# Performance work log

Hardware: AMD Instinct MI355X
Metric: run time of the kernel (lower is better)

The kernel has to match this reference:

```python
import jax, jax.numpy as jnp
import numpy as np

D = 256  # channel dim and CBP output dim


def setup_inputs() -> dict:
    key = jax.random.key(0)
    ks = jax.random.split(key, 14)
    B, C, H, W = 32, 256, 56, 56
    attr_num = 400
    inp = {}
    inp["entity_feature"] = jax.random.normal(ks[0], (B, C, H, W), jnp.float32)
    inp["attr_one_hot"] = jax.random.uniform(ks[1], (B, attr_num), jnp.float32)
    # textual_emb: Linear(attr_num, 256)
    inp["W_emb"] = jax.random.normal(ks[2], (D, attr_num), jnp.float32) * 0.02
    inp["b_emb"] = jnp.zeros((D,), jnp.float32)
    # conv: Conv2d(256,256,1)
    inp["conv_w"] = jax.random.normal(ks[3], (D, D), jnp.float32) * 0.02
    inp["conv_b"] = jnp.zeros((D,), jnp.float32)
    # mcb_conv1_attr: Conv2d(256,32,1)
    inp["conv1_w"] = jax.random.normal(ks[4], (32, D), jnp.float32) * 0.05
    inp["conv1_b"] = jnp.zeros((32,), jnp.float32)
    # mcb_conv2_attr: Conv2d(32,1,1)
    inp["conv2_w"] = jax.random.normal(ks[5], (1, 32), jnp.float32) * 0.1
    inp["conv2_b"] = jnp.zeros((1,), jnp.float32)
    # CompactBilinearPooling count-sketch tables (fixed random at init)
    inp["h1"] = jax.random.randint(ks[6], (D,), 0, D, jnp.int32)
    inp["h2"] = jax.random.randint(ks[7], (D,), 0, D, jnp.int32)
    inp["s1"] = (jax.random.randint(ks[8], (D,), 0, 2, jnp.int32) * 2 - 1).astype(jnp.float32)
    inp["s2"] = (jax.random.randint(ks[9], (D,), 0, 2, jnp.int32) * 2 - 1).astype(jnp.float32)
    return inp


def _sketch_matrix(h, s):
    # sparse count-sketch projection as dense [C_in, D] matrix: P[i, h[i]] = s[i]
    return jnp.zeros((D, D), jnp.float32).at[jnp.arange(D), h].add(s)


def reference(entity_feature, attr_one_hot, W_emb, b_emb, conv_w, conv_b,
              conv1_w, conv1_b, conv2_w, conv2_b, h1, h2, s1, s2):
    feature = jax.nn.relu(entity_feature)                      # [B,256,H,W]
    # textual embedding + spatially-constant 1x1 conv (identical math to
    # expanding then convolving, since the expanded tensor is constant over HxW)
    t = attr_one_hot @ W_emb.T + b_emb                         # [B,256]
    a = t @ conv_w.T + conv_b                                  # [B,256]

    # Compact Bilinear Pooling (count sketch -> FFT -> elementwise mul -> iFFT)
    P1 = _sketch_matrix(h1, s1)
    P2 = _sketch_matrix(h2, s2)
    sk1 = a @ P1                                               # [B,256], spatially constant
    sk2 = jnp.einsum('bchw,cd->bdhw', feature, P2)             # [B,256,H,W]
    fft1 = jnp.fft.rfft(sk1, n=D, axis=1)[:, :, None, None]    # [B,129,1,1]
    fft2 = jnp.fft.rfft(sk2, n=D, axis=1)                      # [B,129,H,W]
    mcb = jnp.fft.irfft(fft1 * fft2, n=D, axis=1)              # [B,256,H,W]

    # gating chain: conv1x1 -> relu -> conv1x1 -> sigmoid
    x = jax.nn.relu(jnp.einsum('bchw,oc->bohw', mcb, conv1_w) + conv1_b[None, :, None, None])
    attr_map = jax.nn.sigmoid(jnp.einsum('bchw,oc->bohw', x, conv2_w) + conv2_b[None, :, None, None])  # [B,1,H,W]
    attr_feature = attr_map * entity_feature                   # [B,256,H,W]
    return attr_map, attr_feature
```

## Files before the change

### kernel.cpp

```cpp
#include <hip/hip_runtime.h>

#define Dq    256
#define ATTR  400
#define HW    3136
#define NB    32
#define PXT   112
#define NPX4  28
#define PITCH 116
#define NTILE 28

typedef __attribute__((ext_vector_type(8))) short bf16x8;
typedef __attribute__((ext_vector_type(4))) float f32x4;

__device__ __forceinline__ unsigned short f2bf(float f) {
  unsigned int x = __float_as_uint(f);
  return (unsigned short)((x + 0x7FFFu + ((x >> 16) & 1u)) >> 16);
}
__device__ __forceinline__ float bf2f(unsigned int u) {
  return __uint_as_float(u << 16);
}

__global__ __launch_bounds__(256) void k_sk1(
    const float* __restrict__ oh, const float* __restrict__ W_emb,
    const float* __restrict__ b_emb, const float* __restrict__ conv_w,
    const float* __restrict__ conv_b, const int* __restrict__ h1,
    const float* __restrict__ s1, float* __restrict__ sk1_out) {
  __shared__ float ohs[ATTR];
  __shared__ float ts[Dq];
  __shared__ float sk[Dq];
  const int b = blockIdx.x, tid = threadIdx.x;
  for (int j = tid; j < ATTR; j += 256) ohs[j] = oh[b * ATTR + j];
  sk[tid] = 0.f;
  __syncthreads();
  float acc = b_emb[tid];
  const float* wr = W_emb + tid * ATTR;
  for (int j = 0; j < ATTR; ++j) acc = fmaf(ohs[j], wr[j], acc);
  ts[tid] = acc;
  __syncthreads();
  float a = conv_b[tid];
  const float* cr = conv_w + tid * Dq;
  for (int k = 0; k < Dq; ++k) a = fmaf(ts[k], cr[k], a);
  atomicAdd(&sk[h1[tid]], a * s1[tid]);
  __syncthreads();
  sk1_out[b * Dq + tid] = sk[tid];
}

__global__ __launch_bounds__(256) void k_G(
    const float* __restrict__ sk1, const float* __restrict__ conv1_w,
    const int* __restrict__ h2, const float* __restrict__ s2,
    unsigned short* __restrict__ Abuf) {
  __shared__ float sks[Dq];
  __shared__ float w1[Dq];
  __shared__ float Tl[Dq];
  const int b = blockIdx.x >> 5, o = blockIdx.x & 31, c = threadIdx.x;
  sks[c] = sk1[b * Dq + c];
  w1[c]  = conv1_w[o * Dq + c];
  __syncthreads();
  float t = 0.f;
  for (int d = 0; d < Dq; ++d) t = fmaf(w1[d], sks[(d - c) & 255], t);
  Tl[c] = t;
  __syncthreads();
  const float g = s2[c] * Tl[h2[c]];
  const int frag = (o >> 4) * 8 + (c >> 5);
  const int lane = (o & 15) | (((c >> 3) & 3) << 4);
  Abuf[(((size_t)b * 16 + frag) * 64 + lane) * 8 + (c & 7)] = f2bf(g);
}

__global__ __launch_bounds__(448, 4) void k_tile(
    const float* __restrict__ ent,
    const unsigned short* __restrict__ Abuf,
    const float* __restrict__ c1b, const float* __restrict__ c2w,
    const float* __restrict__ c2b,
    float* __restrict__ out)
{
  __shared__ unsigned short tile[Dq * PITCH];
  __shared__ float s_lds[PXT];
  const int b = blockIdx.y;
  const int px_base = blockIdx.x * PXT;
  const int t = threadIdx.x;
  const int c0 = t / NPX4;
  const int fi = t % NPX4;

  const float* eb = ent + (size_t)b * Dq * HW + px_base;

#pragma unroll
  for (int k = 0; k < 16; ++k) {
    const int c = 16 * k + c0;
    f32x4 v = *reinterpret_cast<const f32x4*>(eb + (size_t)c * HW + 4 * fi);
    unsigned int d0 = (unsigned int)f2bf(v[0]) | ((unsigned int)f2bf(v[1]) << 16);
    unsigned int d1 = (unsigned int)f2bf(v[2]) | ((unsigned int)f2bf(v[3]) << 16);
    uint2 dv; dv.x = d0; dv.y = d1;
    *reinterpret_cast<uint2*>(&tile[c * PITCH + 4 * fi]) = dv;
  }
  __syncthreads();

  const int w = t >> 6, l = t & 63;
  const int n = l & 15, kg = l >> 4;
  const unsigned short* Ab = Abuf + ((size_t)b * 16 * 64 + l) * 8;

  f32x4 acc0 = {0.f, 0.f, 0.f, 0.f}, acc1 = {0.f, 0.f, 0.f, 0.f};
#pragma unroll
  for (int ks = 0; ks < 8; ++ks) {
    unsigned short uv[8];
#pragma unroll
    for (int j = 0; j < 8; ++j)
      uv[j] = tile[(ks * 32 + kg * 8 + j) * PITCH + w * 16 + n];
    bf16x8 bv;
#pragma unroll
    for (int j = 0; j < 8; ++j)
      bv[j] = (short)((uv[j] & 0x8000u) ? 0u : (unsigned int)uv[j]);
    bf16x8 a0 = *reinterpret_cast<const bf16x8*>(Ab + (size_t)(0 * 8 + ks) * 64 * 8);
    bf16x8 a1 = *reinterpret_cast<const bf16x8*>(Ab + (size_t)(1 * 8 + ks) * 64 * 8);
    acc0 = __builtin_amdgcn_mfma_f32_16x16x32_bf16(a0, bv, acc0, 0, 0, 0);
    acc1 = __builtin_amdgcn_mfma_f32_16x16x32_bf16(a1, bv, acc1, 0, 0, 0);
  }

  const float4 b1a = reinterpret_cast<const float4*>(c1b)[kg];
  const float4 b1b = reinterpret_cast<const float4*>(c1b)[kg + 4];
  const float4 w2a = reinterpret_cast<const float4*>(c2w)[kg];
  const float4 w2b = reinterpret_cast<const float4*>(c2w)[kg + 4];
  float z = 0.f;
  z = fmaf(w2a.x, fmaxf(acc0[0] + b1a.x, 0.f), z);
  z = fmaf(w2a.y, fmaxf(acc0[1] + b1a.y, 0.f), z);
  z = fmaf(w2a.z, fmaxf(acc0[2] + b1a.z, 0.f), z);
  z = fmaf(w2a.w, fmaxf(acc0[3] + b1a.w, 0.f), z);
  z = fmaf(w2b.x, fmaxf(acc1[0] + b1b.x, 0.f), z);
  z = fmaf(w2b.y, fmaxf(acc1[1] + b1b.y, 0.f), z);
  z = fmaf(w2b.z, fmaxf(acc1[2] + b1b.z, 0.f), z);
  z = fmaf(w2b.w, fmaxf(acc1[3] + b1b.w, 0.f), z);
  z += __shfl_xor(z, 16);
  z += __shfl_xor(z, 32);
  const float s = 1.f / (1.f + __expf(-(z + c2b[0])));
  if (l < 16) {
    out[(size_t)b * HW + px_base + w * 16 + l] = s;
    s_lds[w * 16 + l] = s;
  }
  __syncthreads();

  const f32x4 s4 = *reinterpret_cast<const f32x4*>(&s_lds[4 * fi]);
  float* fb = out + (size_t)NB * HW + (size_t)b * Dq * HW + px_base;
#pragma unroll
  for (int k = 0; k < 16; ++k) {
    const int c = 16 * k + c0;
    uint2 dv = *reinterpret_cast<const uint2*>(&tile[c * PITCH + 4 * fi]);
    f32x4 r;
    r[0] = bf2f(dv.x & 0xFFFFu) * s4[0];
    r[1] = bf2f(dv.x >> 16)     * s4[1];
    r[2] = bf2f(dv.y & 0xFFFFu) * s4[2];
    r[3] = bf2f(dv.y >> 16)     * s4[3];
    *reinterpret_cast<f32x4*>(fb + (size_t)c * HW + 4 * fi) = r;
  }
}

extern "C" void kernel_launch(void* const* d_in, const int* in_sizes, int n_in,
                              void* d_out, int out_size, void* d_ws, size_t ws_size,
                              hipStream_t stream) {
  const float* ent    = (const float*)d_in[0];
  const float* oh     = (const float*)d_in[1];
  const float* W_emb  = (const float*)d_in[2];
  const float* b_emb  = (const float*)d_in[3];
  const float* conv_w = (const float*)d_in[4];
  const float* conv_b = (const float*)d_in[5];
  const float* c1w    = (const float*)d_in[6];
  const float* c1b    = (const float*)d_in[7];
  const float* c2w    = (const float*)d_in[8];
  const float* c2b    = (const float*)d_in[9];
  const int*   h1     = (const int*)d_in[10];
  const int*   h2     = (const int*)d_in[11];
  const float* s1     = (const float*)d_in[12];
  const float* s2     = (const float*)d_in[13];

  float* ws  = (float*)d_ws;
  float* sk1 = ws;
  unsigned short* Abuf = (unsigned short*)(ws + NB * Dq);

  hipLaunchKernelGGL(k_sk1, dim3(NB), dim3(256), 0, stream,
                     oh, W_emb, b_emb, conv_w, conv_b, h1, s1, sk1);
  hipLaunchKernelGGL(k_G, dim3(NB * 32), dim3(256), 0, stream,
                     sk1, c1w, h2, s2, Abuf);
  hipLaunchKernelGGL(k_tile, dim3(NTILE, NB), dim3(448), 0, stream,
                     ent, Abuf, c1b, c2w, c2b, (float*)d_out);
}
```

Before: 70.31 us.

## Load entity tile via direct global-to-LDS fp32 copies and shrink pixel tile

The main tile kernel now stages the entity feature tile in LDS as fp32 using global_load_lds direct copies instead of register loads followed by bf16 packing. The tile shrinks to 64 pixels with 256-thread blocks, giving 49 tiles per batch. The bf16 conversion and ReLU move into the MFMA operand build. The output multiply now uses exact fp32 entity values rather than bf16-rounded ones, which also fixes a precision loss in attr_feature. The cost is double the LDS footprint per pixel, fewer pixels per block, and an unpadded layout that may cause bank conflicts in the column-wise MFMA reads.

```diff
diff --git a/kernel.cpp b/kernel.cpp
--- a/kernel.cpp
+++ b/kernel.cpp
@@ -4,10 +4,8 @@
 #define ATTR  400
 #define HW    3136
 #define NB    32
-#define PXT   112
-#define NPX4  28
-#define PITCH 116
-#define NTILE 28
+#define PXT   64
+#define NTILE 49
 
 typedef __attribute__((ext_vector_type(8))) short bf16x8;
 typedef __attribute__((ext_vector_type(4))) float f32x4;
@@ -16,8 +14,12 @@
   unsigned int x = __float_as_uint(f);
   return (unsigned short)((x + 0x7FFFu + ((x >> 16) & 1u)) >> 16);
 }
-__device__ __forceinline__ float bf2f(unsigned int u) {
-  return __uint_as_float(u << 16);
+
+__device__ __forceinline__ void g2lds16(const float* g, float* l) {
+  __builtin_amdgcn_global_load_lds(
+      (const __attribute__((address_space(1))) unsigned int*)g,
+      (__attribute__((address_space(3))) unsigned int*)l,
+      16, 0, 0);
 }
 
 __global__ __launch_bounds__(256) void k_sk1(
@@ -66,49 +68,43 @@
   Abuf[(((size_t)b * 16 + frag) * 64 + lane) * 8 + (c & 7)] = f2bf(g);
 }
 
-__global__ __launch_bounds__(448, 4) void k_tile(
+__global__ __launch_bounds__(256) void k_tile(
     const float* __restrict__ ent,
     const unsigned short* __restrict__ Abuf,
     const float* __restrict__ c1b, const float* __restrict__ c2w,
     const float* __restrict__ c2b,
     float* __restrict__ out)
 {
-  __shared__ unsigned short tile[Dq * PITCH];
+  __shared__ float tile[Dq * PXT];
   __shared__ float s_lds[PXT];
   const int b = blockIdx.y;
   const int px_base = blockIdx.x * PXT;
   const int t = threadIdx.x;
-  const int c0 = t / NPX4;
-  const int fi = t % NPX4;
+  const int w = t >> 6, l = t & 63;
 
   const float* eb = ent + (size_t)b * Dq * HW + px_base;
 
 #pragma unroll
-  for (int k = 0; k < 16; ++k) {
-    const int c = 16 * k + c0;
-    f32x4 v = *reinterpret_cast<const f32x4*>(eb + (size_t)c * HW + 4 * fi);
-    unsigned int d0 = (unsigned int)f2bf(v[0]) | ((unsigned int)f2bf(v[1]) << 16);
-    unsigned int d1 = (unsigned int)f2bf(v[2]) | ((unsigned int)f2bf(v[3]) << 16);
-    uint2 dv; dv.x = d0; dv.y = d1;
-    *reinterpret_cast<uint2*>(&tile[c * PITCH + 4 * fi]) = dv;
+  for (int i = 0; i < 16; ++i) {
+    const int cb = w * 64 + i * 4;
+    const float* src = eb + (size_t)(cb + (l >> 4)) * HW + 4 * (l & 15);
+    g2lds16(src, &tile[cb * PXT]);
   }
+  asm volatile("s_waitcnt vmcnt(0)");
   __syncthreads();
 
-  const int w = t >> 6, l = t & 63;
   const int n = l & 15, kg = l >> 4;
   const unsigned short* Ab = Abuf + ((size_t)b * 16 * 64 + l) * 8;
 
   f32x4 acc0 = {0.f, 0.f, 0.f, 0.f}, acc1 = {0.f, 0.f, 0.f, 0.f};
 #pragma unroll
   for (int ks = 0; ks < 8; ++ks) {
-    unsigned short uv[8];
-#pragma unroll
-    for (int j = 0; j < 8; ++j)
-      uv[j] = tile[(ks * 32 + kg * 8 + j) * PITCH + w * 16 + n];
     bf16x8 bv;
 #pragma unroll
-    for (int j = 0; j < 8; ++j)
-      bv[j] = (short)((uv[j] & 0x8000u) ? 0u : (unsigned int)uv[j]);
+    for (int j = 0; j < 8; ++j) {
+      const float fv = tile[(ks * 32 + kg * 8 + j) * PXT + w * 16 + n];
+      bv[j] = (short)f2bf(fmaxf(fv, 0.f));
+    }
     bf16x8 a0 = *reinterpret_cast<const bf16x8*>(Ab + (size_t)(0 * 8 + ks) * 64 * 8);
     bf16x8 a1 = *reinterpret_cast<const bf16x8*>(Ab + (size_t)(1 * 8 + ks) * 64 * 8);
     acc0 = __builtin_amdgcn_mfma_f32_16x16x32_bf16(a0, bv, acc0, 0, 0, 0);
@@ -137,18 +133,13 @@
   }
   __syncthreads();
 
-  const f32x4 s4 = *reinterpret_cast<const f32x4*>(&s_lds[4 * fi]);
+  const f32x4 s4v = *reinterpret_cast<const f32x4*>(&s_lds[(t & 15) * 4]);
   float* fb = out + (size_t)NB * HW + (size_t)b * Dq * HW + px_base;
 #pragma unroll
   for (int k = 0; k < 16; ++k) {
-    const int c = 16 * k + c0;
-    uint2 dv = *reinterpret_cast<const uint2*>(&tile[c * PITCH + 4 * fi]);
-    f32x4 r;
-    r[0] = bf2f(dv.x & 0xFFFFu) * s4[0];
-    r[1] = bf2f(dv.x >> 16)     * s4[1];
-    r[2] = bf2f(dv.y & 0xFFFFu) * s4[2];
-    r[3] = bf2f(dv.y >> 16)     * s4[3];
-    *reinterpret_cast<f32x4*>(fb + (size_t)c * HW + 4 * fi) = r;
+    const int c = k * 16 + (t >> 4);
+    f32x4 e = *reinterpret_cast<const f32x4*>(&tile[c * PXT + (t & 15) * 4]);
+    *reinterpret_cast<f32x4*>(fb + (size_t)c * HW + (t & 15) * 4) = e * s4v;
   }
 }
 
@@ -178,6 +169,6 @@
                      oh, W_emb, b_emb, conv_w, conv_b, h1, s1, sk1);
   hipLaunchKernelGGL(k_G, dim3(NB * 32), dim3(256), 0, stream,
                      sk1, c1w, h2, s2, Abuf);
-  hipLaunchKernelGGL(k_tile, dim3(NTILE, NB), dim3(448), 0, stream,
+  hipLaunchKernelGGL(k_tile, dim3(NTILE, NB), dim3(256), 0, stream,
                      ent, Abuf, c1b, c2w, c2b, (float*)d_out);
 }
```

Result: slower. 73.22 us (+4.1%).
